# Optimization experiments

Hardware: AMD Instinct MI355X
Metric: run time of the kernel (lower is better)

Reference implementation:

```python
import jax, jax.numpy as jnp
import numpy as np

NOPE, ROPE, VDIM, QKD = 128, 64, 128, 192
H = 16
EPS = 1e-6
SCALING = QKD ** -0.5


def rms_norm(x, w):
    xf = x.astype(jnp.float32)
    var = jnp.mean(xf * xf, axis=-1, keepdims=True)
    return (w * (xf * jax.lax.rsqrt(var + EPS))).astype(x.dtype)


def rotate_half(x):
    d = x.shape[-1] // 2
    return jnp.concatenate((-x[..., d:], x[..., :d]), axis=-1)


def apply_rope(q, k, cos, sin):
    # cos/sin: [B,S,D] -> unsqueeze head dim
    cos = cos[:, None, :, :]
    sin = sin[:, None, :, :]
    return q * cos + rotate_half(q) * sin, k * cos + rotate_half(k) * sin


def setup_inputs() -> dict:
    key = jax.random.key(0)
    ks = jax.random.split(key, 8)
    B, S, D = 2, 2048, 2048
    pos = jnp.arange(S, dtype=jnp.float32)
    inv_freq = 1.0 / (10000.0 ** (jnp.arange(0, ROPE, 2, dtype=jnp.float32) / ROPE))
    ang = pos[:, None] * inv_freq[None, :]            # [S, ROPE/2]
    emb = jnp.concatenate([ang, ang], axis=-1)        # [S, ROPE]
    cos = jnp.broadcast_to(jnp.cos(emb)[None], (B, S, ROPE))
    sin = jnp.broadcast_to(jnp.sin(emb)[None], (B, S, ROPE))
    s = lambda k, shp, fan: jax.random.normal(k, shp, jnp.float32) * (fan ** -0.5)
    return {
        "hidden_states": jax.random.normal(ks[0], (B, S, D), jnp.float32),
        "cos": cos,
        "sin": sin,
        "q_a_W": s(ks[1], (1536, D), D),
        "q_a_norm_w": jnp.ones((1536,), jnp.float32),
        "q_b_W": s(ks[2], (H * QKD, 1536), 1536),
        "kv_a_W": s(ks[3], (512 + ROPE, D), D),
        "kv_a_norm_w": jnp.ones((512,), jnp.float32),
        "kv_b_W": s(ks[4], (H * (NOPE + VDIM), 512), 512),
        "o_W": s(ks[5], (D, H * VDIM), H * VDIM),
    }


def reference(hidden_states, cos, sin, q_a_W, q_a_norm_w, q_b_W, kv_a_W,
              kv_a_norm_w, kv_b_W, o_W):
    B, S, D = hidden_states.shape
    # low-rank Q path
    q = rms_norm(hidden_states @ q_a_W.T, q_a_norm_w) @ q_b_W.T   # [B,S,H*QKD]
    q = q.reshape(B, S, H, QKD).transpose(0, 2, 1, 3)             # [B,H,S,QKD]
    q_pass, q_rot = q[..., :NOPE], q[..., NOPE:]
    # compressed KV path
    ckv = hidden_states @ kv_a_W.T                                # [B,S,512+ROPE]
    k_lat, k_rot = ckv[..., :512], ckv[..., 512:]
    kv = rms_norm(k_lat, kv_a_norm_w) @ kv_b_W.T                  # [B,S,H*(NOPE+VDIM)]
    kv = kv.reshape(B, S, H, NOPE + VDIM).transpose(0, 2, 1, 3)   # [B,H,S,*]
    k_pass, v = kv[..., :NOPE], kv[..., NOPE:]
    k_rot = k_rot.reshape(B, 1, S, ROPE)
    q_rot, k_rot = apply_rope(q_rot, k_rot, cos, sin)
    k_rot = jnp.broadcast_to(k_rot, (B, H, S, ROPE))
    query = jnp.concatenate((q_pass, q_rot), axis=-1)             # [B,H,S,QKD]
    key = jnp.concatenate((k_pass, k_rot), axis=-1)
    # eager causal attention
    scores = jnp.einsum('bhsd,bhtd->bhst', query, key) * SCALING
    causal = jnp.tril(jnp.ones((S, S), bool))
    scores = jnp.where(causal, scores, jnp.finfo(scores.dtype).min)
    attn = jax.nn.softmax(scores.astype(jnp.float32), axis=-1).astype(query.dtype)
    out = jnp.einsum('bhst,bhtd->bhsd', attn, v)                  # [B,H,S,VDIM]
    out = out.transpose(0, 2, 1, 3).reshape(B, S, H * VDIM)
    return out @ o_W.T
```

## Files before the change

### kernel.cpp

```cpp
#include <hip/hip_runtime.h>
#include <hip/hip_bf16.h>


typedef __bf16 bf16x8 __attribute__((ext_vector_type(8)));
typedef float floatx4 __attribute__((ext_vector_type(4)));
#define BF16 __hip_bfloat16

static __device__ __forceinline__ BF16 f2b(float x) { return __float2bfloat16(x); }
static __device__ __forceinline__ unsigned short b2u(BF16 x) { return *(unsigned short*)&x; }
static __device__ __forceinline__ float fast_exp2(float x) { return __builtin_amdgcn_exp2f(x); }

static __device__ __forceinline__ void load_lds16(const BF16* g, BF16* l) {
  __builtin_amdgcn_global_load_lds((__attribute__((address_space(1))) void*)(void*)g,
                                   (__attribute__((address_space(3))) void*)(void*)l,
                                   16, 0, 0);
}

struct CastArgs {
  const float* src[6];
  BF16* dst[6];
  long n[6];
};
__global__ void cast_multi_k(CastArgs a) {
  int r = blockIdx.y;
  long n = a.n[r];
  const float* __restrict__ x = a.src[r];
  BF16* __restrict__ y = a.dst[r];
  for (long i = ((long)blockIdx.x * 256 + threadIdx.x) * 4; i + 3 < n;
       i += (long)gridDim.x * 1024) {
    float4 v = *(const float4*)(x + i);
    y[i+0] = f2b(v.x); y[i+1] = f2b(v.y); y[i+2] = f2b(v.z); y[i+3] = f2b(v.w);
  }
}

template<int OUT_MODE>
__global__ __launch_bounds__(256) void gemm_lds(const BF16* __restrict__ A, const BF16* __restrict__ B,
                                                void* __restrict__ C, int M, int N, int K,
                                                const float* __restrict__ cosb,
                                                const float* __restrict__ sinb,
                                                BF16* __restrict__ P1, BF16* __restrict__ P2) {
  __shared__ __align__(16) BF16 As[128*32];
  __shared__ __align__(16) BF16 Bs[128*32];
  int tid = threadIdx.x, wave = tid >> 6, lane = tid & 63;
  int wr = wave >> 1, wc = wave & 1, lr = lane & 15, quad = lane >> 4;
  long m0 = (long)blockIdx.y * 128, n0 = (long)blockIdx.x * 128;

  int c0 = wave*64 + lane, c1 = c0 + 256;
  const BF16* ga0 = A + (m0 + (c0>>2))*(long)K + (c0&3)*8;
  const BF16* ga1 = A + (m0 + (c1>>2))*(long)K + (c1&3)*8;
  long bn0 = n0 + (c0>>2); if (bn0 >= N) bn0 = N-1;
  long bn1 = n0 + (c1>>2); if (bn1 >= N) bn1 = N-1;
  const BF16* gb0 = B + bn0*(long)K + (c0&3)*8;
  const BF16* gb1 = B + bn1*(long)K + (c1&3)*8;
  BF16* la0 = As + wave*512;
  BF16* la1 = As + wave*512 + 2048;
  BF16* lb0 = Bs + wave*512;
  BF16* lb1 = Bs + wave*512 + 2048;

  floatx4 acc[4][4] = {};
  for (int k0 = 0; k0 < K; k0 += 32) {
    __syncthreads();
    load_lds16(ga0 + k0, la0);
    load_lds16(ga1 + k0, la1);
    load_lds16(gb0 + k0, lb0);
    load_lds16(gb1 + k0, lb1);
    __syncthreads();
    bf16x8 a[4], b[4];
#pragma unroll
    for (int i = 0; i < 4; i++) a[i] = *(const bf16x8*)(As + (wr*64 + i*16 + lr)*32 + quad*8);
#pragma unroll
    for (int j = 0; j < 4; j++) b[j] = *(const bf16x8*)(Bs + (wc*64 + j*16 + lr)*32 + quad*8);
#pragma unroll
    for (int i = 0; i < 4; i++)
#pragma unroll
      for (int j = 0; j < 4; j++)
        acc[i][j] = __builtin_amdgcn_mfma_f32_16x16x32_bf16(a[i], b[j], acc[i][j], 0, 0, 0);
  }

  long n0w = n0 + wc*64;
  const float SCALE_L2E = 0.104117546f;
#pragma unroll
  for (int i = 0; i < 4; i++) {
    long tok = m0 + wr*64 + i*16 + quad*4;
    long bb = tok >> 11, s = tok & 2047;
    if (OUT_MODE == 0) {
#pragma unroll
      for (int r = 0; r < 4; r++) {
        long row = tok + r;
#pragma unroll
        for (int j = 0; j < 4; j++) {
          long col = n0w + j*16 + lr;
          if (col < N) ((float*)C)[row*(long)N + col] = acc[i][j][r];
        }
      }
    } else if (OUT_MODE == 2) {
#pragma unroll
      for (int j = 0; j < 4; j++) {
        long col = n0w + j*16 + lr;
        long h = col >> 8, d = col & 255;
        if (d < 128) {
#pragma unroll
          for (int r = 0; r < 4; r++)
            P1[((bb*16 + h)*2048 + s + r)*192 + d] = f2b(acc[i][j][r]);
        } else {
          ushort4 pk;
          pk.x = b2u(f2b(acc[i][j][0])); pk.y = b2u(f2b(acc[i][j][1]));
          pk.z = b2u(f2b(acc[i][j][2])); pk.w = b2u(f2b(acc[i][j][3]));
          *(ushort4*)(P2 + ((bb*16 + h)*128 + d - 128)*2048 + s) = pk;
        }
      }
    } else {
      bool rope = ((n0w % 192) == 128);
#pragma unroll
      for (int r = 0; r < 4; r++) {
        long row = tok + r;
#pragma unroll
        for (int j = 0; j < 4; j++) {
          long col = n0w + j*16 + lr;
          float x = acc[i][j][r], val;
          if (rope) {
            int id = j*16 + lr;
            float partner = acc[i][j^2][r];
            float rot = (j < 2) ? -partner : partner;
            val = x*cosb[row*64 + id] + rot*sinb[row*64 + id];
          } else {
            val = x;
          }
          long h = col / 192, d = col % 192;
          P1[((bb*16 + h)*2048 + s + r)*192 + d] = f2b(val * SCALE_L2E);
        }
      }
    }
  }
}

template<int D>
__global__ __launch_bounds__(256) void rmsnorm_k(const float* __restrict__ x, const float* __restrict__ w,
                                                 BF16* __restrict__ y, int ld_in, int ld_out) {
  long row = blockIdx.x;
  const float* xr = x + row * (long)ld_in;
  float ss = 0.f;
  for (int i = threadIdx.x * 4; i < D; i += 1024) {
    float4 v = *(const float4*)(xr + i);
    ss += v.x*v.x + v.y*v.y + v.z*v.z + v.w*v.w;
  }
#pragma unroll
  for (int off = 32; off > 0; off >>= 1) ss += __shfl_down(ss, off);
  __shared__ float red[4];
  if ((threadIdx.x & 63) == 0) red[threadIdx.x >> 6] = ss;
  __syncthreads();
  float tot = red[0] + red[1] + red[2] + red[3];
  float rs = rsqrtf(tot / (float)D + 1e-6f);
  BF16* yr = y + row * (long)ld_out;
  for (int i = threadIdx.x * 4; i < D; i += 1024) {
    float4 v = *(const float4*)(xr + i);
    yr[i+0] = f2b(v.x * w[i+0] * rs);
    yr[i+1] = f2b(v.y * w[i+1] * rs);
    yr[i+2] = f2b(v.z * w[i+2] * rs);
    yr[i+3] = f2b(v.w * w[i+3] * rs);
  }
}

__global__ void prep_krot_k(const float* __restrict__ krot, int ld, const float* __restrict__ cosb,
                            const float* __restrict__ sinb, BF16* __restrict__ Kt) {
  long row = blockIdx.x; int i = threadIdx.x;
  const float* kr = krot + row * (long)ld;
  float x = kr[i];
  float rot = (i < 32) ? -kr[i + 32] : kr[i - 32];
  BF16 v = f2b(x * cosb[row*64 + i] + rot * sinb[row*64 + i]);
  long b = row >> 11, s = row & 2047;
  long base = ((b*16)*2048 + s)*192 + 128 + i;
#pragma unroll
  for (int h = 0; h < 16; h++) Kt[base + (long)h*2048*192] = v;
}

#define LK 200
#define LV 72
#define LP 72
__global__ __launch_bounds__(256, 2) void flash_k(const BF16* __restrict__ Qt, const BF16* __restrict__ Kt,
                                                  const BF16* __restrict__ Vt, BF16* __restrict__ O) {
  __shared__ __align__(16) BF16 Ks[64*LK];
  __shared__ __align__(16) BF16 Vs[128*LV];
  __shared__ __align__(16) BF16 Ps[4][16*LP];
  int tid = threadIdx.x, wave = tid >> 6, lane = tid & 63;
  int lr = lane & 15, quad = lane >> 4;
  int F = blockIdx.x;
  int g = F & 31, qti = 15 - (F >> 5);
  int h = g & 15, b = g >> 4;
  const BF16* Qb = Qt + ((long)(b*16 + h) * 2048) * 192;
  const BF16* Kb = Kt + ((long)(b*16 + h) * 2048) * 192;
  const BF16* Vb = Vt + ((long)(b*16 + h) * 128) * 2048;
  const float NEG_INF = -__builtin_inff();
  int q0 = qti * 128;

  int krow[6], kcol[6];
#pragma unroll
  for (int i = 0; i < 6; i++) {
    int c = tid + 256*i;
    krow[i] = c / 24; kcol[i] = (c % 24) * 8;
  }
  int vrow[4], vcol[4];
#pragma unroll
  for (int i = 0; i < 4; i++) {
    int c = tid + 256*i;
    vrow[i] = c >> 3; vcol[i] = (c & 7) * 8;
  }

  bf16x8 kreg[6], vreg[4];
  auto stage_load = [&](int k0) {
#pragma unroll
    for (int i = 0; i < 6; i++)
      kreg[i] = *(const bf16x8*)(Kb + (long)(k0 + krow[i])*192 + kcol[i]);
#pragma unroll
    for (int i = 0; i < 4; i++)
      vreg[i] = *(const bf16x8*)(Vb + (long)vrow[i]*2048 + k0 + vcol[i]);
  };
  auto stage_store = [&]() {
#pragma unroll
    for (int i = 0; i < 6; i++)
      *(bf16x8*)(Ks + krow[i]*LK + kcol[i]) = kreg[i];
#pragma unroll
    for (int i = 0; i < 4; i++)
      *(bf16x8*)(Vs + vrow[i]*LV + vcol[i]) = vreg[i];
  };

  bf16x8 qf[2][6];
#pragma unroll
  for (int s = 0; s < 2; s++) {
    const BF16* qp = Qb + (long)(q0 + s*64 + wave*16 + lr) * 192 + quad*8;
#pragma unroll
    for (int f = 0; f < 6; f++) qf[s][f] = *(const bf16x8*)(qp + f*32);
  }
  float m_i[2][4], l_i[2][4];
#pragma unroll
  for (int s = 0; s < 2; s++)
#pragma unroll
    for (int r = 0; r < 4; r++) { m_i[s][r] = NEG_INF; l_i[s][r] = 0.f; }
  floatx4 o_acc[2][8] = {};

  int nk = 2*qti + 2;
  stage_load(0);
  for (int kt = 0; kt < nk; kt++) {
    int k0 = kt * 64;
    __syncthreads();
    stage_store();
    __syncthreads();
    if (kt + 1 < nk) stage_load(k0 + 64);
#pragma unroll
    for (int s = 0; s < 2; s++) {
      int diag = 2*qti + s;
      if (kt > diag) continue;
      floatx4 st[4];
#pragma unroll
      for (int t = 0; t < 4; t++) {
        floatx4 c = {};
#pragma unroll
        for (int f = 0; f < 6; f++) {
          bf16x8 kf = *(const bf16x8*)(Ks + (t*16+lr)*LK + f*32 + quad*8);
          c = __builtin_amdgcn_mfma_f32_16x16x32_bf16(qf[s][f], kf, c, 0, 0, 0);
        }
        st[t] = c;
      }
      float mt[4];
#pragma unroll
      for (int r = 0; r < 4; r++) mt[r] = NEG_INF;
      if (kt == diag) {
#pragma unroll
        for (int t = 0; t < 4; t++) {
          int coff = t*16 + lr;
#pragma unroll
          for (int r = 0; r < 4; r++) {
            float sc = st[t][r];
            if (coff > wave*16 + quad*4 + r) sc = NEG_INF;
            st[t][r] = sc;
            mt[r] = fmaxf(mt[r], sc);
          }
        }
      } else {
#pragma unroll
        for (int t = 0; t < 4; t++)
#pragma unroll
          for (int r = 0; r < 4; r++) mt[r] = fmaxf(mt[r], st[t][r]);
      }
#pragma unroll
      for (int off = 1; off < 16; off <<= 1)
#pragma unroll
        for (int r = 0; r < 4; r++) mt[r] = fmaxf(mt[r], __shfl_xor(mt[r], off));
      float alpha[4], rsum[4];
#pragma unroll
      for (int r = 0; r < 4; r++) {
        float mn = fmaxf(m_i[s][r], mt[r]);
        alpha[r] = fast_exp2(m_i[s][r] - mn);
        m_i[s][r] = mn;
        rsum[r] = 0.f;
      }
#pragma unroll
      for (int t = 0; t < 4; t++)
#pragma unroll
        for (int r = 0; r < 4; r++) {
          float p = fast_exp2(st[t][r] - m_i[s][r]);
          st[t][r] = p;
          rsum[r] += p;
        }
#pragma unroll
      for (int off = 1; off < 16; off <<= 1)
#pragma unroll
        for (int r = 0; r < 4; r++) rsum[r] += __shfl_xor(rsum[r], off);
#pragma unroll
      for (int r = 0; r < 4; r++) l_i[s][r] = l_i[s][r]*alpha[r] + rsum[r];
#pragma unroll
      for (int v = 0; v < 8; v++)
#pragma unroll
        for (int r = 0; r < 4; r++) o_acc[s][v][r] *= alpha[r];
#pragma unroll
      for (int t = 0; t < 4; t++)
#pragma unroll
        for (int r = 0; r < 4; r++)
          Ps[wave][(quad*4 + r)*LP + t*16 + lr] = f2b(st[t][r]);
#pragma unroll
      for (int kc = 0; kc < 2; kc++) {
        bf16x8 pa = *(const bf16x8*)(&Ps[wave][lr*LP + kc*32 + quad*8]);
#pragma unroll
        for (int v = 0; v < 8; v++) {
          bf16x8 vf = *(const bf16x8*)(&Vs[(v*16+lr)*LV + kc*32 + quad*8]);
          o_acc[s][v] = __builtin_amdgcn_mfma_f32_16x16x32_bf16(pa, vf, o_acc[s][v], 0, 0, 0);
        }
      }
    }
  }
#pragma unroll
  for (int s = 0; s < 2; s++) {
    long rowb = q0 + s*64 + wave*16 + quad*4;
#pragma unroll
    for (int v = 0; v < 8; v++)
#pragma unroll
      for (int r = 0; r < 4; r++) {
        long row = rowb + r;
        O[((long)b*2048 + row)*2048 + h*128 + v*16 + lr] = f2b(o_acc[s][v][r] / l_i[s][r]);
      }
  }
}

extern "C" void kernel_launch(void* const* d_in, const int* in_sizes, int n_in,
                              void* d_out, int out_size, void* d_ws, size_t ws_size,
                              hipStream_t stream) {
  const float* hidden      = (const float*)d_in[0];
  const float* cosb        = (const float*)d_in[1];
  const float* sinb        = (const float*)d_in[2];
  const float* q_a_W       = (const float*)d_in[3];
  const float* q_a_norm_w  = (const float*)d_in[4];
  const float* q_b_W       = (const float*)d_in[5];
  const float* kv_a_W      = (const float*)d_in[6];
  const float* kv_a_norm_w = (const float*)d_in[7];
  const float* kv_b_W      = (const float*)d_in[8];
  const float* o_W         = (const float*)d_in[9];
  float* out = (float*)d_out;

  const int Mrows = 4096;

  char* ws = (char*)d_ws; size_t off = 0;
  auto alloc = [&](size_t bytes) -> void* {
    void* p = ws + off; off = (off + bytes + 255) & ~(size_t)255; return p;
  };
  BF16* hb    = (BF16*)alloc((size_t)4096*2048*2);
  BF16* Wqakv = (BF16*)alloc((size_t)2112*2048*2);
  BF16* Wqb   = (BF16*)alloc((size_t)3072*1536*2);
  BF16* Wkvb  = (BF16*)alloc((size_t)4096*512*2);
  BF16* Wo    = (BF16*)alloc((size_t)2048*2048*2);
  float* qakv = (float*)alloc((size_t)4096*2112*4);
  BF16* qan   = (BF16*)alloc((size_t)4096*1536*2);
  BF16* kvn   = (BF16*)alloc((size_t)4096*512*2);
  BF16* Qt    = (BF16*)alloc((size_t)2*16*2048*192*2);
  BF16* Kt    = (BF16*)alloc((size_t)2*16*2048*192*2);
  BF16* Vt    = (BF16*)alloc((size_t)2*16*128*2048*2);
  BF16* attn  = (BF16*)alloc((size_t)4096*2048*2);

  CastArgs ca;
  ca.src[0] = hidden;  ca.dst[0] = hb;                 ca.n[0] = (long)4096*2048;
  ca.src[1] = q_a_W;   ca.dst[1] = Wqakv;              ca.n[1] = (long)1536*2048;
  ca.src[2] = kv_a_W;  ca.dst[2] = Wqakv + (long)1536*2048; ca.n[2] = (long)576*2048;
  ca.src[3] = q_b_W;   ca.dst[3] = Wqb;                ca.n[3] = (long)3072*1536;
  ca.src[4] = kv_b_W;  ca.dst[4] = Wkvb;               ca.n[4] = (long)4096*512;
  ca.src[5] = o_W;     ca.dst[5] = Wo;                 ca.n[5] = (long)2048*2048;
  cast_multi_k<<<dim3(1024, 6), dim3(256), 0, stream>>>(ca);

  gemm_lds<0><<<dim3(17, 32), dim3(256), 0, stream>>>(hb, Wqakv, qakv, Mrows, 2112, 2048,
                                                      nullptr, nullptr, nullptr, nullptr);
  rmsnorm_k<1536><<<dim3(4096), dim3(256), 0, stream>>>(qakv, q_a_norm_w, qan, 2112, 1536);
  rmsnorm_k<512><<<dim3(4096), dim3(256), 0, stream>>>(qakv + 1536, kv_a_norm_w, kvn, 2112, 512);
  prep_krot_k<<<dim3(4096), dim3(64), 0, stream>>>(qakv + 2048, 2112, cosb, sinb, Kt);

  gemm_lds<3><<<dim3(24, 32), dim3(256), 0, stream>>>(qan, Wqb, nullptr, Mrows, 3072, 1536,
                                                      cosb, sinb, Qt, nullptr);
  gemm_lds<2><<<dim3(32, 32), dim3(256), 0, stream>>>(kvn, Wkvb, nullptr, Mrows, 4096, 512,
                                                      nullptr, nullptr, Kt, Vt);

  flash_k<<<dim3(512), dim3(256), 0, stream>>>(Qt, Kt, Vt, attn);

  gemm_lds<0><<<dim3(16, 32), dim3(256), 0, stream>>>(attn, Wo, out, Mrows, 2048, 2048,
                                                      nullptr, nullptr, nullptr, nullptr);
}
```

Baseline: 543.4 us.

## Split flash tile into 64-row halves paired for balanced causal work

Each block now handles two 64-row query tiles in sequence, tile j and tile 31-j, instead of one 128-row tile spanning two sub-tiles. Every block therefore does the same total amount of causal work, which removes the load imbalance of the old largest-first schedule. The cost is that K/V tiles are no longer shared between two query sub-tiles, so K/V traffic per query row roughly doubles. The launch-bounds minimum-blocks hint is also dropped, which changes how the compiler budgets registers.

Result: faster. 490.4 us (-9.8%).

```diff
diff --git a/kernel.cpp b/kernel.cpp
--- a/kernel.cpp
+++ b/kernel.cpp
@@ -177,21 +177,20 @@
 #define LK 200
 #define LV 72
 #define LP 72
-__global__ __launch_bounds__(256, 2) void flash_k(const BF16* __restrict__ Qt, const BF16* __restrict__ Kt,
-                                                  const BF16* __restrict__ Vt, BF16* __restrict__ O) {
+__global__ __launch_bounds__(256) void flash_k(const BF16* __restrict__ Qt, const BF16* __restrict__ Kt,
+                                               const BF16* __restrict__ Vt, BF16* __restrict__ O) {
   __shared__ __align__(16) BF16 Ks[64*LK];
   __shared__ __align__(16) BF16 Vs[128*LV];
   __shared__ __align__(16) BF16 Ps[4][16*LP];
   int tid = threadIdx.x, wave = tid >> 6, lane = tid & 63;
   int lr = lane & 15, quad = lane >> 4;
   int F = blockIdx.x;
-  int g = F & 31, qti = 15 - (F >> 5);
+  int g = F & 31, jidx = F >> 5;
   int h = g & 15, b = g >> 4;
   const BF16* Qb = Qt + ((long)(b*16 + h) * 2048) * 192;
   const BF16* Kb = Kt + ((long)(b*16 + h) * 2048) * 192;
   const BF16* Vb = Vt + ((long)(b*16 + h) * 128) * 2048;
   const float NEG_INF = -__builtin_inff();
-  int q0 = qti * 128;
 
   int krow[6], kcol[6];
 #pragma unroll
@@ -224,32 +223,26 @@
       *(bf16x8*)(Vs + vrow[i]*LV + vcol[i]) = vreg[i];
   };
 
-  bf16x8 qf[2][6];
-#pragma unroll
-  for (int s = 0; s < 2; s++) {
-    const BF16* qp = Qb + (long)(q0 + s*64 + wave*16 + lr) * 192 + quad*8;
-#pragma unroll
-    for (int f = 0; f < 6; f++) qf[s][f] = *(const bf16x8*)(qp + f*32);
-  }
-  float m_i[2][4], l_i[2][4];
-#pragma unroll
-  for (int s = 0; s < 2; s++)
-#pragma unroll
-    for (int r = 0; r < 4; r++) { m_i[s][r] = NEG_INF; l_i[s][r] = 0.f; }
-  floatx4 o_acc[2][8] = {};
-
-  int nk = 2*qti + 2;
-  stage_load(0);
-  for (int kt = 0; kt < nk; kt++) {
-    int k0 = kt * 64;
-    __syncthreads();
-    stage_store();
-    __syncthreads();
-    if (kt + 1 < nk) stage_load(k0 + 64);
-#pragma unroll
-    for (int s = 0; s < 2; s++) {
-      int diag = 2*qti + s;
-      if (kt > diag) continue;
+  for (int half = 0; half < 2; half++) {
+    int qt = (half == 0) ? jidx : 31 - jidx;
+    int q0 = qt * 64;
+    bf16x8 qf[6];
+    {
+      const BF16* qp = Qb + (long)(q0 + wave*16 + lr) * 192 + quad*8;
+#pragma unroll
+      for (int f = 0; f < 6; f++) qf[f] = *(const bf16x8*)(qp + f*32);
+    }
+    float m_i[4], l_i[4];
+#pragma unroll
+    for (int r = 0; r < 4; r++) { m_i[r] = NEG_INF; l_i[r] = 0.f; }
+    floatx4 o_acc[8] = {};
+    int nk = qt + 1;
+    stage_load(0);
+    for (int kt = 0; kt < nk; kt++) {
+      __syncthreads();
+      stage_store();
+      __syncthreads();
+      if (kt + 1 < nk) stage_load((kt + 1) * 64);
       floatx4 st[4];
 #pragma unroll
       for (int t = 0; t < 4; t++) {
@@ -257,14 +250,14 @@
 #pragma unroll
         for (int f = 0; f < 6; f++) {
           bf16x8 kf = *(const bf16x8*)(Ks + (t*16+lr)*LK + f*32 + quad*8);
-          c = __builtin_amdgcn_mfma_f32_16x16x32_bf16(qf[s][f], kf, c, 0, 0, 0);
+          c = __builtin_amdgcn_mfma_f32_16x16x32_bf16(qf[f], kf, c, 0, 0, 0);
         }
         st[t] = c;
       }
       float mt[4];
 #pragma unroll
       for (int r = 0; r < 4; r++) mt[r] = NEG_INF;
-      if (kt == diag) {
+      if (kt == qt) {
 #pragma unroll
         for (int t = 0; t < 4; t++) {
           int coff = t*16 + lr;
@@ -289,16 +282,16 @@
       float alpha[4], rsum[4];
 #pragma unroll
       for (int r = 0; r < 4; r++) {
-        float mn = fmaxf(m_i[s][r], mt[r]);
-        alpha[r] = fast_exp2(m_i[s][r] - mn);
-        m_i[s][r] = mn;
+        float mn = fmaxf(m_i[r], mt[r]);
+        alpha[r] = fast_exp2(m_i[r] - mn);
+        m_i[r] = mn;
         rsum[r] = 0.f;
       }
 #pragma unroll
       for (int t = 0; t < 4; t++)
 #pragma unroll
         for (int r = 0; r < 4; r++) {
-          float p = fast_exp2(st[t][r] - m_i[s][r]);
+          float p = fast_exp2(st[t][r] - m_i[r]);
           st[t][r] = p;
           rsum[r] += p;
         }
@@ -307,11 +300,11 @@
 #pragma unroll
         for (int r = 0; r < 4; r++) rsum[r] += __shfl_xor(rsum[r], off);
 #pragma unroll
-      for (int r = 0; r < 4; r++) l_i[s][r] = l_i[s][r]*alpha[r] + rsum[r];
+      for (int r = 0; r < 4; r++) l_i[r] = l_i[r]*alpha[r] + rsum[r];
 #pragma unroll
       for (int v = 0; v < 8; v++)
 #pragma unroll
-        for (int r = 0; r < 4; r++) o_acc[s][v][r] *= alpha[r];
+        for (int r = 0; r < 4; r++) o_acc[v][r] *= alpha[r];
 #pragma unroll
       for (int t = 0; t < 4; t++)
 #pragma unroll
@@ -323,20 +316,17 @@
 #pragma unroll
         for (int v = 0; v < 8; v++) {
           bf16x8 vf = *(const bf16x8*)(&Vs[(v*16+lr)*LV + kc*32 + quad*8]);
-          o_acc[s][v] = __builtin_amdgcn_mfma_f32_16x16x32_bf16(pa, vf, o_acc[s][v], 0, 0, 0);
+          o_acc[v] = __builtin_amdgcn_mfma_f32_16x16x32_bf16(pa, vf, o_acc[v], 0, 0, 0);
         }
       }
     }
-  }
-#pragma unroll
-  for (int s = 0; s < 2; s++) {
-    long rowb = q0 + s*64 + wave*16 + quad*4;
+    long rowb = q0 + wave*16 + quad*4;
 #pragma unroll
     for (int v = 0; v < 8; v++)
 #pragma unroll
       for (int r = 0; r < 4; r++) {
         long row = rowb + r;
-        O[((long)b*2048 + row)*2048 + h*128 + v*16 + lr] = f2b(o_acc[s][v][r] / l_i[s][r]);
+        O[((long)b*2048 + row)*2048 + h*128 + v*16 + lr] = f2b(o_acc[v][r] / l_i[r]);
       }
   }
 }
```
